# Kernel optimization log

Measured on AMD Instinct MI355X. Metric: run time of the kernel, lower is better.

Reference implementation:

```python
import jax, jax.numpy as jnp
import numpy as np

DEPTH = 6
N_LEAF = 2 ** DEPTH          # 64
GATE_COUNT = N_LEAF - 1      # 63
IN_F = 512
OUT_F = 512
BATCH = 1024


def setup_inputs() -> dict:
    key = jax.random.key(0)
    k1, k2, k3 = jax.random.split(key, 3)
    x = jax.random.normal(k1, (BATCH, IN_F), dtype=jnp.float32)
    gw = jax.random.normal(k2, (IN_F, GATE_COUNT), dtype=jnp.float32)
    gb = jnp.zeros((GATE_COUNT,), dtype=jnp.float32)
    pw = jax.random.normal(k3, (OUT_F, IN_F, N_LEAF), dtype=jnp.float32)
    pb = jnp.zeros((OUT_F, N_LEAF), dtype=jnp.float32)
    return {"x": x, "gw": gw, "gb": gb, "pw": pw, "pb": pb}


def _leaf_probs(x, gw, gb, depth):
    # gatings: sigmoid(x @ gw + gb), shape [B, gate_count]
    g = jax.nn.sigmoid(x @ gw + gb)
    B = x.shape[0]
    dens = jnp.ones((B, 1), dtype=x.dtype)  # root density
    offset = 0
    for d in range(depth):
        n = 2 ** d
        gp = g[:, offset:offset + n]                    # parent gatings [B, n]
        # left child multiplies by g, right child by (1 - g), interleaved
        pair = jnp.stack([gp, 1.0 - gp], axis=-1).reshape(B, 2 * n)
        dens = jnp.repeat(dens, 2, axis=1) * pair        # [B, 2n]
        offset += n
    return dens  # [B, n_leaf]


def reference(x, gw, gb, pw, pb):
    leaf = _leaf_probs(x, gw, gb, DEPTH)                 # [B, L]
    # per-leaf linear projections, then mix with leaf probabilities
    y = jnp.einsum('bi,oil->bol', x, pw)                 # [B, O, L]
    out = jnp.einsum('bol,bl->bo', y, leaf) + leaf @ pb.T
    return out
```

## Files before the change

kernel.cpp:

```cpp
#include <hip/hip_runtime.h>
#include <hip/hip_bf16.h>

#define TDEPTH 6
#define NLEAF 64
#define NGATE 63
#define INF 512
#define OUTF 512
#define BATCH 1024

#define BM 256
#define BN 128
#define SPLITK 16
#define KCH 513
#define THREADS 512
#define XPITCH 36

typedef __attribute__((ext_vector_type(4))) float f32x4;
typedef __attribute__((ext_vector_type(4))) __bf16 bf16x4;
typedef __attribute__((ext_vector_type(8))) __bf16 bf16x8;

__global__ __launch_bounds__(256) void leaf_kernel(
    const float* __restrict__ x, const float* __restrict__ gw,
    const float* __restrict__ gb, float* __restrict__ leaf) {
  const int wid = threadIdx.x >> 6, lane = threadIdx.x & 63;
  const int b = blockIdx.x * 4 + wid;
  __shared__ float g[4][NLEAF];
  if (lane < NGATE) {
    const float* xr = x + (size_t)b * INF;
    float a0 = 0.f, a1 = 0.f, a2 = 0.f, a3 = 0.f;
    #pragma unroll 4
    for (int i = 0; i < INF; i += 4) {
      a0 += xr[i + 0] * gw[(i + 0) * NGATE + lane];
      a1 += xr[i + 1] * gw[(i + 1) * NGATE + lane];
      a2 += xr[i + 2] * gw[(i + 2) * NGATE + lane];
      a3 += xr[i + 3] * gw[(i + 3) * NGATE + lane];
    }
    float t = (a0 + a1) + (a2 + a3) + gb[lane];
    g[wid][lane] = 1.0f / (1.0f + __expf(-t));
  }
  __syncthreads();
  float p = 1.0f;
  #pragma unroll
  for (int d = 0; d < TDEPTH; d++) {
    int prefix = lane >> (TDEPTH - 1 - d);
    int node = (1 << d) - 1 + (prefix >> 1);
    float gv = g[wid][node];
    p *= (prefix & 1) ? (1.0f - gv) : gv;
  }
  leaf[(size_t)b * NLEAF + lane] = p;
}

__device__ __forceinline__ void load_b4(f32x4 (&bv)[4], const float* src) {
  #pragma unroll
  for (int j = 0; j < 4; j++) bv[j] = *(const f32x4*)(src + j * 16);
}

__device__ __forceinline__ void store_b(__bf16* Bb, int bo, int c,
                                        const f32x4 (&bv)[4]) {
  const int swz = (bo & 7) << 4;
  #pragma unroll
  for (int j = 0; j < 4; j++) {
    bf16x4 w;
    w[0] = (__bf16)bv[j][0]; w[1] = (__bf16)bv[j][1];
    w[2] = (__bf16)bv[j][2]; w[3] = (__bf16)bv[j][3];
    int byte = bo * 128 + ((c * 8 + j * 32) ^ swz);
    *(bf16x4*)((char*)Bb + byte) = w;
  }
}

__global__ __launch_bounds__(THREADS, 2) void gemm_kernel(
    const float* __restrict__ x, const float* __restrict__ pw,
    const float* __restrict__ pb, const float* __restrict__ leaf,
    float* __restrict__ partial) {
  __shared__ float xsm[BM * XPITCH];
  __shared__ __bf16 Bsm[2][BN * 64];

  const int tid = threadIdx.x;
  const int lane = tid & 63;
  const int wid = tid >> 6;
  const int wm = wid >> 1, wn = wid & 1;
  const int q = lane >> 4, rl = lane & 15;

  const int bid = blockIdx.x;
  const int L = (bid & 7) * 32 + (bid >> 3);
  const int mb = L & 3, g = L >> 2;
  const int nb = g >> 4, s = g & 15;
  const int m0 = mb * BM, n0 = nb * BN;
  const int cs = (s * KCH) / SPLITK;
  const int ce = ((s + 1) * KCH) / SPLITK;
  const int nreal = min(ce, INF) - cs;
  const bool bias_tile = (ce == KCH);

  f32x4 lf[4][2][2];
  #pragma unroll
  for (int mi = 0; mi < 4; mi++) {
    const float* lr = leaf + (size_t)(m0 + wm * 64 + mi * 16 + rl) * NLEAF + q * 8;
    #pragma unroll
    for (int kk = 0; kk < 2; kk++) {
      lf[mi][kk][0] = *(const f32x4*)(lr + kk * 32);
      lf[mi][kk][1] = *(const f32x4*)(lr + kk * 32 + 4);
    }
  }

  {
    int r = tid >> 1, h = tid & 1;
    const float* src = x + (size_t)(m0 + r) * INF + cs + h * 16;
    float* dst = xsm + r * XPITCH + h * 16;
    #pragma unroll
    for (int j = 0; j < 4; j++) *(f32x4*)(dst + j * 4) = *(const f32x4*)(src + j * 4);
  }

  const int bo = tid >> 2;
  const int bc = tid & 3;
  const float* pwrow = pw + (size_t)(n0 + bo) * (INF * NLEAF) + bc * 4;
  const float* pbrow = pb + (size_t)(n0 + bo) * NLEAF + bc * 4;

  f32x4 acc[4][4];
  #pragma unroll
  for (int mi = 0; mi < 4; mi++)
    #pragma unroll
    for (int ni = 0; ni < 4; ni++) acc[mi][ni] = (f32x4){0.f, 0.f, 0.f, 0.f};

  f32x4 bv[4];
  load_b4(bv, pwrow + (size_t)cs * NLEAF);
  store_b(Bsm[0], bo, bc, bv);
  __syncthreads();

  #pragma unroll 2
  for (int t = 0; t < nreal; t++) {
    const int cur = t & 1, nxt = cur ^ 1;
    const bool more = (t + 1 < nreal) || bias_tile;
    const bool next_is_bias = (t + 1 >= nreal);
    if (more) {
      if (!next_is_bias) load_b4(bv, pwrow + (size_t)(cs + t + 1) * NLEAF);
      else               load_b4(bv, pbrow);
    }
    float xv[4];
    #pragma unroll
    for (int mi = 0; mi < 4; mi++)
      xv[mi] = xsm[(wm * 64 + mi * 16 + rl) * XPITCH + t];
    #pragma unroll
    for (int kk = 0; kk < 2; kk++) {
      bf16x8 bfr[4];
      #pragma unroll
      for (int ni = 0; ni < 4; ni++) {
        int row = wn * 64 + ni * 16 + rl;
        int byte = row * 128 + ((kk * 64 + q * 16) ^ ((row & 7) << 4));
        bfr[ni] = *(const bf16x8*)((const char*)Bsm[cur] + byte);
      }
      #pragma unroll
      for (int mi = 0; mi < 4; mi++) {
        f32x4 p0 = lf[mi][kk][0] * xv[mi];
        f32x4 p1 = lf[mi][kk][1] * xv[mi];
        bf16x8 a;
        a[0] = (__bf16)p0[0]; a[1] = (__bf16)p0[1];
        a[2] = (__bf16)p0[2]; a[3] = (__bf16)p0[3];
        a[4] = (__bf16)p1[0]; a[5] = (__bf16)p1[1];
        a[6] = (__bf16)p1[2]; a[7] = (__bf16)p1[3];
        #pragma unroll
        for (int ni = 0; ni < 4; ni++)
          acc[mi][ni] = __builtin_amdgcn_mfma_f32_16x16x32_bf16(
              a, bfr[ni], acc[mi][ni], 0, 0, 0);
      }
    }
    if (more) store_b(Bsm[nxt], bo, bc, bv);
    __syncthreads();
  }

  if (bias_tile) {
    const int cur = nreal & 1;
    #pragma unroll
    for (int kk = 0; kk < 2; kk++) {
      bf16x8 bfr[4];
      #pragma unroll
      for (int ni = 0; ni < 4; ni++) {
        int row = wn * 64 + ni * 16 + rl;
        int byte = row * 128 + ((kk * 64 + q * 16) ^ ((row & 7) << 4));
        bfr[ni] = *(const bf16x8*)((const char*)Bsm[cur] + byte);
      }
      #pragma unroll
      for (int mi = 0; mi < 4; mi++) {
        f32x4 p0 = lf[mi][kk][0], p1 = lf[mi][kk][1];
        bf16x8 a;
        a[0] = (__bf16)p0[0]; a[1] = (__bf16)p0[1];
        a[2] = (__bf16)p0[2]; a[3] = (__bf16)p0[3];
        a[4] = (__bf16)p1[0]; a[5] = (__bf16)p1[1];
        a[6] = (__bf16)p1[2]; a[7] = (__bf16)p1[3];
        #pragma unroll
        for (int ni = 0; ni < 4; ni++)
          acc[mi][ni] = __builtin_amdgcn_mfma_f32_16x16x32_bf16(
              a, bfr[ni], acc[mi][ni], 0, 0, 0);
      }
    }
  }

  float* dst = partial + ((size_t)s * BATCH + m0) * OUTF + n0;
  #pragma unroll
  for (int mi = 0; mi < 4; mi++)
    #pragma unroll
    for (int ni = 0; ni < 4; ni++)
      #pragma unroll
      for (int r = 0; r < 4; r++) {
        int row = wm * 64 + mi * 16 + q * 4 + r;
        int col = wn * 64 + ni * 16 + rl;
        dst[(size_t)row * OUTF + col] = acc[mi][ni][r];
      }
}

__global__ __launch_bounds__(256) void reduce_kernel(
    const float* __restrict__ partial, float* __restrict__ out) {
  size_t e = ((size_t)blockIdx.x * 256 + threadIdx.x) * 4;
  f32x4 sum = (f32x4){0.f, 0.f, 0.f, 0.f};
  #pragma unroll
  for (int s = 0; s < SPLITK; s++)
    sum += *(const f32x4*)(partial + (size_t)s * BATCH * OUTF + e);
  *(f32x4*)(out + e) = sum;
}

extern "C" void kernel_launch(void* const* d_in, const int* in_sizes, int n_in,
                              void* d_out, int out_size, void* d_ws, size_t ws_size,
                              hipStream_t stream) {
  const float* x  = (const float*)d_in[0];
  const float* gw = (const float*)d_in[1];
  const float* gb = (const float*)d_in[2];
  const float* pw = (const float*)d_in[3];
  const float* pb = (const float*)d_in[4];
  float* out = (float*)d_out;

  float* leaf    = (float*)d_ws;
  float* partial = (float*)((char*)d_ws + (1 << 19));

  leaf_kernel<<<BATCH / 4, 256, 0, stream>>>(x, gw, gb, leaf);
  gemm_kernel<<<(BATCH / BM) * (OUTF / BN) * SPLITK, THREADS, 0, stream>>>(
      x, pw, pb, leaf, partial);
  reduce_kernel<<<(BATCH * OUTF) / (256 * 4), 256, 0, stream>>>(partial, out);
}
```

Before: 72.62 us.

## Deepen B prefetch to two stages with padded LDS and raw barriers

```diff
diff --git a/kernel.cpp b/kernel.cpp
--- a/kernel.cpp
+++ b/kernel.cpp
@@ -14,9 +14,9 @@
 #define KCH 513
 #define THREADS 512
 #define XPITCH 36
+#define BPITCH 144
 
 typedef __attribute__((ext_vector_type(4))) float f32x4;
-typedef __attribute__((ext_vector_type(4))) __bf16 bf16x4;
 typedef __attribute__((ext_vector_type(8))) __bf16 bf16x8;
 
 __global__ __launch_bounds__(256) void leaf_kernel(
@@ -50,30 +50,19 @@
   leaf[(size_t)b * NLEAF + lane] = p;
 }
 
-__device__ __forceinline__ void load_b4(f32x4 (&bv)[4], const float* src) {
-  #pragma unroll
-  for (int j = 0; j < 4; j++) bv[j] = *(const f32x4*)(src + j * 16);
-}
-
-__device__ __forceinline__ void store_b(__bf16* Bb, int bo, int c,
-                                        const f32x4 (&bv)[4]) {
-  const int swz = (bo & 7) << 4;
-  #pragma unroll
-  for (int j = 0; j < 4; j++) {
-    bf16x4 w;
-    w[0] = (__bf16)bv[j][0]; w[1] = (__bf16)bv[j][1];
-    w[2] = (__bf16)bv[j][2]; w[3] = (__bf16)bv[j][3];
-    int byte = bo * 128 + ((c * 8 + j * 32) ^ swz);
-    *(bf16x4*)((char*)Bb + byte) = w;
-  }
+__device__ __forceinline__ void sync_raw() {
+  asm volatile("s_waitcnt lgkmcnt(0)" ::: "memory");
+  __builtin_amdgcn_sched_barrier(0);
+  __builtin_amdgcn_s_barrier();
+  __builtin_amdgcn_sched_barrier(0);
 }
 
 __global__ __launch_bounds__(THREADS, 2) void gemm_kernel(
     const float* __restrict__ x, const float* __restrict__ pw,
     const float* __restrict__ pb, const float* __restrict__ leaf,
     float* __restrict__ partial) {
-  __shared__ float xsm[BM * XPITCH];
-  __shared__ __bf16 Bsm[2][BN * 64];
+  __shared__ __align__(16) float xsm[BM * XPITCH];
+  __shared__ __align__(16) __bf16 Bsm[2][BN * (BPITCH / 2)];
 
   const int tid = threadIdx.x;
   const int lane = tid & 63;
@@ -89,7 +78,7 @@
   const int cs = (s * KCH) / SPLITK;
   const int ce = ((s + 1) * KCH) / SPLITK;
   const int nreal = min(ce, INF) - cs;
-  const bool bias_tile = (ce == KCH);
+  const int total = nreal + ((ce == KCH) ? 1 : 0);
 
   f32x4 lf[4][2][2];
   #pragma unroll
@@ -102,51 +91,70 @@
     }
   }
 
+  const int bo = tid >> 2, bc = tid & 3;
+  const float* pwrow = pw + (size_t)(n0 + bo) * (INF * NLEAF) + bc * 16;
+  const float* pbrow = pb + (size_t)(n0 + bo) * NLEAF + bc * 16;
+
+  f32x4 acc[4][4];
+  #pragma unroll
+  for (int mi = 0; mi < 4; mi++)
+    #pragma unroll
+    for (int ni = 0; ni < 4; ni++) acc[mi][ni] = (f32x4){0.f, 0.f, 0.f, 0.f};
+
+  f32x4 bvA[4], bvB[4];
+
+  {
+    const float* s0 = pwrow + (size_t)cs * NLEAF;
+    #pragma unroll
+    for (int j = 0; j < 4; j++) bvA[j] = *(const f32x4*)(s0 + j * 4);
+    const float* s1 = pwrow + (size_t)(cs + 1) * NLEAF;
+    #pragma unroll
+    for (int j = 0; j < 4; j++) bvB[j] = *(const f32x4*)(s1 + j * 4);
+  }
   {
     int r = tid >> 1, h = tid & 1;
     const float* src = x + (size_t)(m0 + r) * INF + cs + h * 16;
     float* dst = xsm + r * XPITCH + h * 16;
     #pragma unroll
-    for (int j = 0; j < 4; j++) *(f32x4*)(dst + j * 4) = *(const f32x4*)(src + j * 4);
-  }
-
-  const int bo = tid >> 2;
-  const int bc = tid & 3;
-  const float* pwrow = pw + (size_t)(n0 + bo) * (INF * NLEAF) + bc * 4;
-  const float* pbrow = pb + (size_t)(n0 + bo) * NLEAF + bc * 4;
-
-  f32x4 acc[4][4];
-  #pragma unroll
-  for (int mi = 0; mi < 4; mi++)
-    #pragma unroll
-    for (int ni = 0; ni < 4; ni++) acc[mi][ni] = (f32x4){0.f, 0.f, 0.f, 0.f};
-
-  f32x4 bv[4];
-  load_b4(bv, pwrow + (size_t)cs * NLEAF);
-  store_b(Bsm[0], bo, bc, bv);
-  __syncthreads();
-
-  #pragma unroll 2
-  for (int t = 0; t < nreal; t++) {
-    const int cur = t & 1, nxt = cur ^ 1;
-    const bool more = (t + 1 < nreal) || bias_tile;
-    const bool next_is_bias = (t + 1 >= nreal);
-    if (more) {
-      if (!next_is_bias) load_b4(bv, pwrow + (size_t)(cs + t + 1) * NLEAF);
-      else               load_b4(bv, pbrow);
+    for (int j = 0; j < 4; j++)
+      *(f32x4*)(dst + j * 4) = *(const f32x4*)(src + j * 4);
+  }
+  {
+    #pragma unroll
+    for (int h = 0; h < 2; h++) {
+      f32x4 lo = bvA[2 * h], hi = bvA[2 * h + 1];
+      bf16x8 w;
+      w[0] = (__bf16)lo[0]; w[1] = (__bf16)lo[1];
+      w[2] = (__bf16)lo[2]; w[3] = (__bf16)lo[3];
+      w[4] = (__bf16)hi[0]; w[5] = (__bf16)hi[1];
+      w[6] = (__bf16)hi[2]; w[7] = (__bf16)hi[3];
+      *(bf16x8*)((char*)&Bsm[0][0] + bo * BPITCH + bc * 32 + h * 16) = w;
+    }
+  }
+  sync_raw();
+
+  auto step_body = [&](int t, f32x4(&Rld)[4], f32x4(&Rst)[4],
+                       __bf16* cur, __bf16* nxt) {
+    if (t + 2 < total) {
+      const float* s2 = (t + 2 < nreal)
+          ? pwrow + (size_t)(cs + t + 2) * NLEAF : pbrow;
+      #pragma unroll
+      for (int j = 0; j < 4; j++) Rld[j] = *(const f32x4*)(s2 + j * 4);
     }
     float xv[4];
     #pragma unroll
-    for (int mi = 0; mi < 4; mi++)
-      xv[mi] = xsm[(wm * 64 + mi * 16 + rl) * XPITCH + t];
+    for (int mi = 0; mi < 4; mi++) {
+      float v = xsm[(wm * 64 + mi * 16 + rl) * XPITCH + (t & 31)];
+      xv[mi] = (t < nreal) ? v : 1.0f;
+    }
     #pragma unroll
     for (int kk = 0; kk < 2; kk++) {
       bf16x8 bfr[4];
       #pragma unroll
       for (int ni = 0; ni < 4; ni++) {
         int row = wn * 64 + ni * 16 + rl;
-        int byte = row * 128 + ((kk * 64 + q * 16) ^ ((row & 7) << 4));
-        bfr[ni] = *(const bf16x8*)((const char*)Bsm[cur] + byte);
+        bfr[ni] = *(const bf16x8*)((const char*)cur + row * BPITCH +
+                                   kk * 64 + q * 16);
       }
       #pragma unroll
       for (int mi = 0; mi < 4; mi++) {
@@ -163,35 +171,26 @@
               a, bfr[ni], acc[mi][ni], 0, 0, 0);
       }
     }
-    if (more) store_b(Bsm[nxt], bo, bc, bv);
-    __syncthreads();
-  }
-
-  if (bias_tile) {
-    const int cur = nreal & 1;
-    #pragma unroll
-    for (int kk = 0; kk < 2; kk++) {
-      bf16x8 bfr[4];
-      #pragma unroll
-      for (int ni = 0; ni < 4; ni++) {
-        int row = wn * 64 + ni * 16 + rl;
-        int byte = row * 128 + ((kk * 64 + q * 16) ^ ((row & 7) << 4));
-        bfr[ni] = *(const bf16x8*)((const char*)Bsm[cur] + byte);
-      }
-      #pragma unroll
-      for (int mi = 0; mi < 4; mi++) {
-        f32x4 p0 = lf[mi][kk][0], p1 = lf[mi][kk][1];
-        bf16x8 a;
-        a[0] = (__bf16)p0[0]; a[1] = (__bf16)p0[1];
-        a[2] = (__bf16)p0[2]; a[3] = (__bf16)p0[3];
-        a[4] = (__bf16)p1[0]; a[5] = (__bf16)p1[1];
-        a[6] = (__bf16)p1[2]; a[7] = (__bf16)p1[3];
-        #pragma unroll
-        for (int ni = 0; ni < 4; ni++)
-          acc[mi][ni] = __builtin_amdgcn_mfma_f32_16x16x32_bf16(
-              a, bfr[ni], acc[mi][ni], 0, 0, 0);
-      }
-    }
+    if (t + 1 < total) {
+      #pragma unroll
+      for (int h = 0; h < 2; h++) {
+        f32x4 lo = Rst[2 * h], hi = Rst[2 * h + 1];
+        bf16x8 w;
+        w[0] = (__bf16)lo[0]; w[1] = (__bf16)lo[1];
+        w[2] = (__bf16)lo[2]; w[3] = (__bf16)lo[3];
+        w[4] = (__bf16)hi[0]; w[5] = (__bf16)hi[1];
+        w[6] = (__bf16)hi[2]; w[7] = (__bf16)hi[3];
+        *(bf16x8*)((char*)nxt + bo * BPITCH + bc * 32 + h * 16) = w;
+      }
+    }
+    sync_raw();
+  };
+
+  __bf16* B0 = &Bsm[0][0];
+  __bf16* B1 = &Bsm[1][0];
+  for (int t = 0; t < total; t += 2) {
+    step_body(t, bvA, bvB, B0, B1);
+    if (t + 1 < total) step_body(t + 1, bvB, bvA, B1, B0);
   }
 
   float* dst = partial + ((size_t)s * BATCH + m0) * OUTF + n0;
```

Result: no change. 72.34 us (-0.4%).
